# Optimization experiments

Measured on AMD Instinct MI355X. Metric: run time of the kernel, lower is better.

The kernel has to match this reference:

```python
import jax, jax.numpy as jnp
from jax import lax
import numpy as np

IOU_THRESHOLD = 0.35
SCORE_THRESHOLD = 0.5


def _pairwise_iou(b):
    # b: [N,4] boxes in (ymin, xmin, ymax, xmax) convention (tf boxes)
    y1, x1, y2, x2 = b[:, 0], b[:, 1], b[:, 2], b[:, 3]
    area = (y2 - y1) * (x2 - x1)
    iy1 = jnp.maximum(y1[:, None], y1[None, :])
    ix1 = jnp.maximum(x1[:, None], x1[None, :])
    iy2 = jnp.minimum(y2[:, None], y2[None, :])
    ix2 = jnp.minimum(x2[:, None], x2[None, :])
    inter = jnp.maximum(iy2 - iy1, 0.0) * jnp.maximum(ix2 - ix1, 0.0)
    union = area[:, None] + area[None, :] - inter
    return jnp.where(union > 0, inter / union, 0.0)  # [N,N]


def _nms_sample_image(scores, boxes, anchors_wh, num_samples):
    # scores [N], boxes [N,4], anchors_wh [N,2]
    N = scores.shape[0]
    order = jnp.argsort(-scores)  # descending by score, like tf NMS
    s = scores[order]
    b = boxes[order]
    a = anchors_wh[order]
    valid = s > SCORE_THRESHOLD
    iou = _pairwise_iou(b)  # [N,N] on score-sorted boxes
    idx = jnp.arange(N)

    # greedy suppression: box i kept iff valid and no earlier kept box overlaps > thr
    def step(keep, i):
        suppressed = jnp.any(keep & (idx < i) & (iou[i] > IOU_THRESHOLD))
        return keep.at[i].set(valid[i] & ~suppressed), None

    keep, _ = lax.scan(step, jnp.zeros(N, dtype=bool), idx)

    # gather kept entries in (descending-score) order, then pad/slice to num_samples
    rank = jnp.cumsum(keep) - 1  # output slot for each kept entry
    slot = jnp.where(keep, jnp.minimum(rank, num_samples), num_samples)
    vals = jnp.concatenate([s[:, None], b, a], axis=1)  # [N,7]
    out = jnp.zeros((num_samples + 1, 7), vals.dtype).at[slot].set(vals)
    return out[:num_samples]  # [num_samples, 7] = (score | box(4) | anchor_wh(2))


def reference(scores, boxes, anchors, num_samples):
    # scores [B,H,W,1], boxes [B,H,W,4], anchors [B,H,W,4] (last 2 chans = w,h)
    B = scores.shape[0]
    sc = scores.reshape(B, -1)
    bx = boxes.reshape(B, -1, 4)
    an = anchors[..., 2:].reshape(B, -1, 2)
    out = jax.vmap(lambda s, b, a: _nms_sample_image(s, b, a, num_samples))(sc, bx, an)
    return out  # [B, num_samples, 7]


def setup_inputs() -> dict:
    key = jax.random.key(0)
    k1, k2, k3, k4, k5 = jax.random.split(key, 5)
    B, H, W = 8, 64, 64
    scores = jax.random.uniform(k1, (B, H, W, 1), dtype=jnp.float32)
    # well-formed tf boxes: ymin<ymax, xmin<xmax in [0,1]
    ymin = jax.random.uniform(k2, (B, H, W, 1), dtype=jnp.float32) * 0.8
    xmin = jax.random.uniform(k3, (B, H, W, 1), dtype=jnp.float32) * 0.8
    hh = jax.random.uniform(k4, (B, H, W, 1), dtype=jnp.float32) * 0.18 + 0.02
    ww = jax.random.uniform(k5, (B, H, W, 1), dtype=jnp.float32) * 0.18 + 0.02
    boxes = jnp.concatenate([ymin, xmin, ymin + hh, xmin + ww], axis=-1)
    # anchors: [cy, cx, w, h]-style; only last two channels are used
    k6 = jax.random.fold_in(key, 6)
    anchors = jax.random.uniform(k6, (B, H, W, 4), dtype=jnp.float32) * 0.25 + 0.05
    return {"scores": scores, "boxes": boxes, "anchors": anchors, "num_samples": 300}
```

## Files before the change

### kernel.cpp

```cpp
#include <hip/hip_runtime.h>

static constexpr float kIouT = 0.35f;
static constexpr float kScoreT = 0.5f;
static constexpr int kMaxKeep = 512;

__device__ __forceinline__ float iou_f(const float4 a, const float4 b) {
  float areaA = __fmul_rn(a.z - a.x, a.w - a.y);
  float areaB = __fmul_rn(b.z - b.x, b.w - b.y);
  float iy1 = fmaxf(a.x, b.x);
  float ix1 = fmaxf(a.y, b.y);
  float iy2 = fminf(a.z, b.z);
  float ix2 = fminf(a.w, b.w);
  float dy = fmaxf(iy2 - iy1, 0.0f);
  float dx = fmaxf(ix2 - ix1, 0.0f);
  float inter = __fmul_rn(dy, dx);
  float uni = (areaA + areaB) - inter;
  return (uni > 0.0f) ? __fdiv_rn(inter, uni) : 0.0f;
}

__device__ __forceinline__ unsigned long long rdlane64(unsigned long long v,
                                                       int l) {
  unsigned lo = (unsigned)__builtin_amdgcn_readlane((int)(unsigned)v, l);
  unsigned hi = (unsigned)__builtin_amdgcn_readlane((int)(unsigned)(v >> 32), l);
  return ((unsigned long long)hi << 32) | lo;
}

__global__ __launch_bounds__(256)
void nms_rank_kernel(const float* __restrict__ scores,
                     const float4* __restrict__ boxes,
                     unsigned long long* __restrict__ skeys,
                     float4* __restrict__ sboxes,
                     int* __restrict__ Mcnt, int N, int rankBlocks) {
  const int tid = threadIdx.x;
  const int lane = tid & 63;
  if ((int)blockIdx.x >= rankBlocks) {
    __shared__ int part[4];
    const int img = blockIdx.x - rankBlocks;
    const int wv = tid >> 6;
    const float4* sc4 = (const float4*)(scores + (size_t)img * N);
    int c = 0;
    for (int q = tid; q < (N >> 2); q += 256) {
      float4 v = sc4[q];
      c += (v.x > kScoreT) + (v.y > kScoreT) + (v.z > kScoreT) + (v.w > kScoreT);
    }
#pragma unroll
    for (int off = 1; off < 64; off <<= 1) c += __shfl_xor(c, off, 64);
    if (lane == 0) part[wv] = c;
    __syncthreads();
    if (tid == 0) Mcnt[img] = part[0] + part[1] + part[2] + part[3];
    return;
  }
  const int wid = (int)(((unsigned)blockIdx.x * blockDim.x + tid) >> 6);
  const int img = wid / N;
  const int row = wid - img * N;
  const float* sc = scores + (size_t)img * N;
  const float si = sc[row];
  if (!(si > kScoreT)) return;
  const float4* sc4 = (const float4*)sc;
  int cnt = 0;
  for (int q = lane; q < (N >> 2); q += 64) {
    const float4 v = sc4[q];
    const int j = q << 2;
    cnt += (v.x > si) + (v.y > si) + (v.z > si) + (v.w > si);
    if (v.x == si && j < row) cnt++;
    if (v.y == si && j + 1 < row) cnt++;
    if (v.z == si && j + 2 < row) cnt++;
    if (v.w == si && j + 3 < row) cnt++;
  }
#pragma unroll
  for (int off = 1; off < 64; off <<= 1) cnt += __shfl_xor(cnt, off, 64);
  if (lane == 0) {
    skeys[(size_t)img * N + cnt] =
        ((unsigned long long)(~__float_as_uint(si)) << 32) | (unsigned)row;
    sboxes[(size_t)img * N + cnt] = boxes[(size_t)img * N + row];
  }
}

__global__ __launch_bounds__(256)
void nms_mask_kernel(const float4* __restrict__ sboxes,
                     const int* __restrict__ Mcnt,
                     unsigned long long* __restrict__ mask,
                     int N, int totalRows) {
  const int wid = (int)(((unsigned)blockIdx.x * blockDim.x + threadIdx.x) >> 6);
  const int lane = threadIdx.x & 63;
  if (wid >= totalRows) return;
  const int img = wid / N;
  const int row = wid - img * N;
  const int m = Mcnt[img];
  if (row >= m) return;
  const float4* sb = sboxes + (size_t)img * N;
  const float4 bi = sb[row];
  const int nw = (m + 63) >> 6;
  unsigned long long* mrow = mask + (size_t)wid * (size_t)(N >> 6);
  for (int w = row >> 6; w < nw; ++w) {
    int j = (w << 6) | lane;
    bool sup = false;
    if (j > row && j < m) sup = iou_f(bi, sb[j]) > kIouT;
    unsigned long long bm = __ballot(sup);
    if (lane == 0) mrow[w] = bm;
  }
}

__global__ __launch_bounds__(64)
void nms_scan_kernel(const unsigned long long* __restrict__ skeys,
                     const float4* __restrict__ sboxes,
                     const int* __restrict__ Mcnt,
                     const unsigned long long* __restrict__ mask,
                     const float* __restrict__ anchors,
                     float* __restrict__ out, int N, int NS) {
  __shared__ int keptlist[kMaxKeep];
  const int img = blockIdx.x;
  const int lane = threadIdx.x;
  int m = Mcnt[img];
  if (m > N) m = N;
  const int nw = (m + 63) >> 6;
  const int stride = N >> 6;
  const unsigned long long* mbase = mask + (size_t)img * (size_t)N * stride;
  const unsigned long long* kg = skeys + (size_t)img * N;
  const float4* sb = sboxes + (size_t)img * N;
  const float* an = anchors + (size_t)img * (size_t)N * 4;
  float* o = out + (size_t)img * NS * 7;

  int kept = 0;
  unsigned long long remv = 0ull;

  if (m > 0) {
    auto dgload = [&](int cc) -> unsigned long long {
      return (cc < nw) ? mbase[(size_t)((cc << 6) + lane) * stride + cc] : 0ull;
    };
    unsigned long long dg0 = dgload(0);
    unsigned long long dg1 = dgload(1);
    unsigned long long dg2 = dgload(2);

    for (int c = 0; c < nw && kept < NS; ++c) {
      const int cb = c << 6;
      unsigned long long local = rdlane64(remv, c);
      const int rem = m - cb;
      unsigned long long avail = ~local;
      if (rem < 64) avail &= (1ull << rem) - 1ull;
      unsigned long long keptbits = 0ull;
      while (avail != 0ull && kept < NS) {
        const int b = (int)__builtin_ctzll(avail);
        if (lane == 0) keptlist[kept] = cb + b;
        kept++;
        keptbits |= 1ull << b;
        const unsigned long long rc = rdlane64(dg0, b);
        local |= rc;
        avail &= ~local;
        avail &= ~(1ull << b);
      }
      dg0 = dg1; dg1 = dg2; dg2 = dgload(c + 3);
      const bool lok = (lane > c) && (lane < nw);
      while (keptbits != 0ull) {
        unsigned long long t[8];
        int bs[8];
#pragma unroll
        for (int k = 0; k < 8; ++k) {
          if (keptbits != 0ull) {
            bs[k] = (int)__builtin_ctzll(keptbits);
            keptbits &= keptbits - 1ull;
          } else {
            bs[k] = -1;
          }
        }
#pragma unroll
        for (int k = 0; k < 8; ++k)
          t[k] = (bs[k] >= 0 && lok)
                     ? mbase[(size_t)(cb + bs[k]) * stride + lane]
                     : 0ull;
#pragma unroll
        for (int k = 0; k < 8; ++k)
          if (bs[k] >= 0) remv |= t[k];
      }
    }
  }

  __syncthreads();
  for (int t = lane; t < kept; t += 64) {
    const int i = keptlist[t];
    const unsigned long long ki = kg[i];
    const float4 bi = sb[i];
    const unsigned idx = (unsigned)ki;
    float* row = o + t * 7;
    row[0] = __uint_as_float(~(unsigned)(ki >> 32));
    row[1] = bi.x; row[2] = bi.y; row[3] = bi.z; row[4] = bi.w;
    row[5] = an[idx * 4 + 2];
    row[6] = an[idx * 4 + 3];
  }
  for (int t = kept * 7 + lane; t < NS * 7; t += 64) o[t] = 0.0f;
}

__global__ __launch_bounds__(1024)
void nms_fused_kernel(const float* __restrict__ scores,
                      const float4* __restrict__ boxes,
                      const float* __restrict__ anchors,
                      float* __restrict__ out, int N, int NS) {
  __shared__ unsigned long long keys[4096];
  __shared__ int s_m;
  if (N > 4096) return;
  const int img = blockIdx.x;
  const int tid = threadIdx.x;
  const float* sc = scores + (size_t)img * N;
  const float4* bx = boxes + (size_t)img * N;
  if (tid == 0) s_m = 0;
  __syncthreads();
  int cnt = 0;
  for (int i = tid; i < N; i += blockDim.x) {
    float s = sc[i];
    keys[i] = ((unsigned long long)(~__float_as_uint(s)) << 32) | (unsigned)i;
    if (s > kScoreT) cnt++;
  }
  if (cnt) atomicAdd(&s_m, cnt);
  __syncthreads();
  for (int k = 2; k <= N; k <<= 1) {
    for (int j = k >> 1; j > 0; j >>= 1) {
      for (int i = tid; i < N; i += blockDim.x) {
        int ixj = i ^ j;
        if (ixj > i) {
          unsigned long long a = keys[i];
          unsigned long long b = keys[ixj];
          bool up = ((i & k) == 0);
          if (up ? (a > b) : (a < b)) { keys[i] = b; keys[ixj] = a; }
        }
      }
      __syncthreads();
    }
  }
  if (tid >= 64) return;
  const int lane = tid;
  const int m = s_m;
  const int nw = (m + 63) >> 6;
  const float* an = anchors + (size_t)img * N * 4;
  float* o = out + (size_t)img * NS * 7;
  unsigned long long remv = 0ull;
  int kept = 0;
  for (int i = 0; i < m && kept < NS; ++i) {
    unsigned long long rw = __shfl(remv, i >> 6, 64);
    if ((rw >> (i & 63)) & 1ull) continue;
    unsigned long long ki = keys[i];
    float4 bi = bx[(unsigned)ki];
    if (lane == 0) {
      unsigned idx = (unsigned)ki;
      float* row = o + kept * 7;
      row[0] = __uint_as_float(~(unsigned)(ki >> 32));
      row[1] = bi.x; row[2] = bi.y; row[3] = bi.z; row[4] = bi.w;
      row[5] = an[idx * 4 + 2];
      row[6] = an[idx * 4 + 3];
    }
    kept++;
    for (int w2 = i >> 6; w2 < nw; ++w2) {
      int j = (w2 << 6) | lane;
      bool sup = false;
      if (j > i && j < m) sup = iou_f(bi, bx[(unsigned)keys[j]]) > kIouT;
      unsigned long long bm = __ballot(sup);
      if (lane == w2) remv |= bm;
    }
  }
  for (int t = kept * 7 + lane; t < NS * 7; t += 64) o[t] = 0.0f;
}

extern "C" void kernel_launch(void* const* d_in, const int* in_sizes, int n_in,
                              void* d_out, int out_size, void* d_ws, size_t ws_size,
                              hipStream_t stream) {
  const float* scores = (const float*)d_in[0];
  const float4* boxes = (const float4*)d_in[1];
  const float* anchors = (const float*)d_in[2];
  float* out = (float*)d_out;
  const int B = 8;
  const int N = in_sizes[0] / B;
  const int NS = out_size / (B * 7);

  const size_t nTot = (size_t)B * (size_t)N;
  const size_t keysB = nTot * 8;
  const size_t sboxB = nTot * 16;
  const size_t mcntB = 256;
  const size_t maskB = nTot * (size_t)(N >> 6) * 8;
  const size_t need = keysB + sboxB + mcntB + maskB;

  if (ws_size >= need && (N % 256) == 0 && N >= 256 && N <= 4096 &&
      NS <= kMaxKeep) {
    char* p = (char*)d_ws;
    unsigned long long* skeys = (unsigned long long*)p; p += keysB;
    float4* sboxes = (float4*)p;                         p += sboxB;
    int* Mcnt = (int*)p;                                 p += mcntB;
    unsigned long long* mask = (unsigned long long*)p;

    const int totalRows = B * N;
    const int rankBlocks = totalRows / 4;
    nms_rank_kernel<<<rankBlocks + B, 256, 0, stream>>>(scores, boxes, skeys,
                                                        sboxes, Mcnt, N,
                                                        rankBlocks);
    nms_mask_kernel<<<rankBlocks, 256, 0, stream>>>(sboxes, Mcnt, mask, N,
                                                    totalRows);
    nms_scan_kernel<<<B, 64, 0, stream>>>(skeys, sboxes, Mcnt, mask, anchors,
                                          out, N, NS);
  } else {
    nms_fused_kernel<<<B, 1024, 0, stream>>>(scores, boxes, anchors, out, N, NS);
  }
}
```

Baseline: 108.2 us.

## Replace precomputed NMS mask with on-the-fly chunked suppression in one block per image

Drops the full pairwise IoU bitmask kernel and the mask-based scan, and adds a single 512-thread block per image. Each thread holds up to eight candidate boxes in registers. The block processes 64-box chunks: it resolves in-chunk suppression through a shared diagonal mask, then each thread tests its surviving boxes only against newly kept boxes. This removes the O(N^2) mask write and read traffic and one kernel launch, and stops early once NS boxes are kept. In exchange, the greedy scan is serialized through several block barriers per chunk. The IoU test also gains an early exit for boxes that do not intersect.

```diff
diff --git a/kernel.cpp b/kernel.cpp
--- a/kernel.cpp
+++ b/kernel.cpp
@@ -4,18 +4,16 @@
 static constexpr float kScoreT = 0.5f;
 static constexpr int kMaxKeep = 512;
 
-__device__ __forceinline__ float iou_f(const float4 a, const float4 b) {
-  float areaA = __fmul_rn(a.z - a.x, a.w - a.y);
-  float areaB = __fmul_rn(b.z - b.x, b.w - b.y);
-  float iy1 = fmaxf(a.x, b.x);
-  float ix1 = fmaxf(a.y, b.y);
-  float iy2 = fminf(a.z, b.z);
-  float ix2 = fminf(a.w, b.w);
-  float dy = fmaxf(iy2 - iy1, 0.0f);
-  float dx = fmaxf(ix2 - ix1, 0.0f);
-  float inter = __fmul_rn(dy, dx);
-  float uni = (areaA + areaB) - inter;
-  return (uni > 0.0f) ? __fdiv_rn(inter, uni) : 0.0f;
+__device__ __forceinline__ bool iou_gt(const float4 a, const float4 b) {
+  const float iy1 = fmaxf(a.x, b.x), ix1 = fmaxf(a.y, b.y);
+  const float iy2 = fminf(a.z, b.z), ix2 = fminf(a.w, b.w);
+  const float dy = iy2 - iy1, dx = ix2 - ix1;
+  if (!(dy > 0.0f && dx > 0.0f)) return false;
+  const float inter = __fmul_rn(dy, dx);
+  const float aA = __fmul_rn(a.z - a.x, a.w - a.y);
+  const float aB = __fmul_rn(b.z - b.x, b.w - b.y);
+  const float uni = (aA + aB) - inter;
+  return (uni > 0.0f) && (__fdiv_rn(inter, uni) > kIouT);
 }
 
 __device__ __forceinline__ unsigned long long rdlane64(unsigned long long v,
@@ -76,107 +74,111 @@
   }
 }
 
-__global__ __launch_bounds__(256)
-void nms_mask_kernel(const float4* __restrict__ sboxes,
-                     const int* __restrict__ Mcnt,
-                     unsigned long long* __restrict__ mask,
-                     int N, int totalRows) {
-  const int wid = (int)(((unsigned)blockIdx.x * blockDim.x + threadIdx.x) >> 6);
-  const int lane = threadIdx.x & 63;
-  if (wid >= totalRows) return;
-  const int img = wid / N;
-  const int row = wid - img * N;
-  const int m = Mcnt[img];
-  if (row >= m) return;
-  const float4* sb = sboxes + (size_t)img * N;
-  const float4 bi = sb[row];
-  const int nw = (m + 63) >> 6;
-  unsigned long long* mrow = mask + (size_t)wid * (size_t)(N >> 6);
-  for (int w = row >> 6; w < nw; ++w) {
-    int j = (w << 6) | lane;
-    bool sup = false;
-    if (j > row && j < m) sup = iou_f(bi, sb[j]) > kIouT;
-    unsigned long long bm = __ballot(sup);
-    if (lane == 0) mrow[w] = bm;
-  }
-}
-
-__global__ __launch_bounds__(64)
-void nms_scan_kernel(const unsigned long long* __restrict__ skeys,
+__global__ __launch_bounds__(512, 1)
+void nms_keep_kernel(const unsigned long long* __restrict__ skeys,
                      const float4* __restrict__ sboxes,
                      const int* __restrict__ Mcnt,
-                     const unsigned long long* __restrict__ mask,
                      const float* __restrict__ anchors,
                      float* __restrict__ out, int N, int NS) {
+  __shared__ float4 keptbox[kMaxKeep];
   __shared__ int keptlist[kMaxKeep];
+  __shared__ float4 chunkbox[64];
+  __shared__ unsigned long long smask[64];
+  __shared__ unsigned long long s_ca;
+  __shared__ int s_kept;
   const int img = blockIdx.x;
-  const int lane = threadIdx.x;
+  const int tid = threadIdx.x;
+  const int lane = tid & 63;
+  const int wv = tid >> 6;
   int m = Mcnt[img];
   if (m > N) m = N;
-  const int nw = (m + 63) >> 6;
-  const int stride = N >> 6;
-  const unsigned long long* mbase = mask + (size_t)img * (size_t)N * stride;
+  if (m < 0) m = 0;
   const unsigned long long* kg = skeys + (size_t)img * N;
   const float4* sb = sboxes + (size_t)img * N;
   const float* an = anchors + (size_t)img * (size_t)N * 4;
   float* o = out + (size_t)img * NS * 7;
 
+  float4 obox[8];
+  unsigned alivebits = 0u;
+#pragma unroll
+  for (int k = 0; k < 8; ++k) {
+    const int idx = tid + (k << 9);
+    if (idx < m) { obox[k] = sb[idx]; alivebits |= 1u << k; }
+  }
+  if (tid == 0) s_kept = 0;
+  __syncthreads();
+
   int kept = 0;
-  unsigned long long remv = 0ull;
-
-  if (m > 0) {
-    auto dgload = [&](int cc) -> unsigned long long {
-      return (cc < nw) ? mbase[(size_t)((cc << 6) + lane) * stride + cc] : 0ull;
-    };
-    unsigned long long dg0 = dgload(0);
-    unsigned long long dg1 = dgload(1);
-    unsigned long long dg2 = dgload(2);
-
-    for (int c = 0; c < nw && kept < NS; ++c) {
-      const int cb = c << 6;
-      unsigned long long local = rdlane64(remv, c);
-      const int rem = m - cb;
-      unsigned long long avail = ~local;
-      if (rem < 64) avail &= (1ull << rem) - 1ull;
-      unsigned long long keptbits = 0ull;
-      while (avail != 0ull && kept < NS) {
-        const int b = (int)__builtin_ctzll(avail);
-        if (lane == 0) keptlist[kept] = cb + b;
-        kept++;
-        keptbits |= 1ull << b;
-        const unsigned long long rc = rdlane64(dg0, b);
-        local |= rc;
-        avail &= ~local;
-        avail &= ~(1ull << b);
-      }
-      dg0 = dg1; dg1 = dg2; dg2 = dgload(c + 3);
-      const bool lok = (lane > c) && (lane < nw);
-      while (keptbits != 0ull) {
-        unsigned long long t[8];
-        int bs[8];
-#pragma unroll
-        for (int k = 0; k < 8; ++k) {
-          if (keptbits != 0ull) {
-            bs[k] = (int)__builtin_ctzll(keptbits);
-            keptbits &= keptbits - 1ull;
-          } else {
-            bs[k] = -1;
+  for (int base = 0; base < m && kept < NS; base += 64) {
+    const int ow = (base >> 6) & 7;
+    const int slot = base >> 9;
+    if (wv == ow) {
+      float4 cb = obox[0];
+#pragma unroll
+      for (int k = 1; k < 8; ++k)
+        if (k == slot) cb = obox[k];
+      chunkbox[lane] = cb;
+      const bool al = (alivebits >> slot) & 1u;
+      const unsigned long long bm = __ballot(al);
+      if (lane == 0) s_ca = bm;
+      alivebits &= ~(1u << slot);
+    }
+    __syncthreads();
+    const unsigned long long ca = s_ca;
+    if (ca != 0ull) {
+      const int kbase = kept;
+      {
+        const float4 cj = chunkbox[lane];
+#pragma unroll
+        for (int r = 0; r < 8; ++r) {
+          const int row = (wv << 3) + r;
+          const float4 bi = chunkbox[row];
+          bool sup = false;
+          if (lane > row) sup = iou_gt(bi, cj);
+          const unsigned long long bm = __ballot(sup);
+          if (lane == 0) smask[row] = bm;
+        }
+      }
+      __syncthreads();
+      if (wv == 0) {
+        const unsigned long long diag = smask[lane];
+        unsigned long long avail = ca;
+        unsigned long long local = 0ull, keptbits = 0ull;
+        int kc = kept;
+        while (avail != 0ull && kc < NS) {
+          const int b = (int)__builtin_ctzll(avail);
+          keptbits |= 1ull << b;
+          kc++;
+          local |= rdlane64(diag, b);
+          avail &= ~local;
+          avail &= ~(1ull << b);
+        }
+        if ((keptbits >> lane) & 1ull) {
+          const int rk =
+              (int)__builtin_popcountll(keptbits & ((1ull << lane) - 1ull));
+          keptlist[kbase + rk] = base + lane;
+          keptbox[kbase + rk] = chunkbox[lane];
+        }
+        if (lane == 0) s_kept = kc;
+      }
+      __syncthreads();
+      kept = s_kept;
+      if (kept > kbase && alivebits != 0u) {
+        for (int kk = kbase; kk < kept; ++kk) {
+          const float4 bx = keptbox[kk];
+#pragma unroll
+          for (int k = 0; k < 8; ++k) {
+            if ((alivebits >> k) & 1u) {
+              if (iou_gt(bx, obox[k])) alivebits &= ~(1u << k);
+            }
           }
         }
-#pragma unroll
-        for (int k = 0; k < 8; ++k)
-          t[k] = (bs[k] >= 0 && lok)
-                     ? mbase[(size_t)(cb + bs[k]) * stride + lane]
-                     : 0ull;
-#pragma unroll
-        for (int k = 0; k < 8; ++k)
-          if (bs[k] >= 0) remv |= t[k];
-      }
-    }
-  }
-
-  __syncthreads();
-  for (int t = lane; t < kept; t += 64) {
+      }
+    }
+    __syncthreads();
+  }
+
+  for (int t = tid; t < kept; t += 512) {
     const int i = keptlist[t];
     const unsigned long long ki = kg[i];
     const float4 bi = sb[i];
@@ -187,7 +189,7 @@
     row[5] = an[idx * 4 + 2];
     row[6] = an[idx * 4 + 3];
   }
-  for (int t = kept * 7 + lane; t < NS * 7; t += 64) o[t] = 0.0f;
+  for (int t = kept * 7 + tid; t < NS * 7; t += 512) o[t] = 0.0f;
 }
 
 __global__ __launch_bounds__(1024)
@@ -251,7 +253,7 @@
     for (int w2 = i >> 6; w2 < nw; ++w2) {
       int j = (w2 << 6) | lane;
       bool sup = false;
-      if (j > i && j < m) sup = iou_f(bi, bx[(unsigned)keys[j]]) > kIouT;
+      if (j > i && j < m) sup = iou_gt(bi, bx[(unsigned)keys[j]]);
       unsigned long long bm = __ballot(sup);
       if (lane == w2) remv |= bm;
     }
@@ -274,26 +276,22 @@
   const size_t keysB = nTot * 8;
   const size_t sboxB = nTot * 16;
   const size_t mcntB = 256;
-  const size_t maskB = nTot * (size_t)(N >> 6) * 8;
-  const size_t need = keysB + sboxB + mcntB + maskB;
+  const size_t need = keysB + sboxB + mcntB;
 
   if (ws_size >= need && (N % 256) == 0 && N >= 256 && N <= 4096 &&
       NS <= kMaxKeep) {
     char* p = (char*)d_ws;
     unsigned long long* skeys = (unsigned long long*)p; p += keysB;
     float4* sboxes = (float4*)p;                         p += sboxB;
-    int* Mcnt = (int*)p;                                 p += mcntB;
-    unsigned long long* mask = (unsigned long long*)p;
+    int* Mcnt = (int*)p;
 
     const int totalRows = B * N;
     const int rankBlocks = totalRows / 4;
     nms_rank_kernel<<<rankBlocks + B, 256, 0, stream>>>(scores, boxes, skeys,
                                                         sboxes, Mcnt, N,
                                                         rankBlocks);
-    nms_mask_kernel<<<rankBlocks, 256, 0, stream>>>(sboxes, Mcnt, mask, N,
-                                                    totalRows);
-    nms_scan_kernel<<<B, 64, 0, stream>>>(skeys, sboxes, Mcnt, mask, anchors,
-                                          out, N, NS);
+    nms_keep_kernel<<<B, 512, 0, stream>>>(skeys, sboxes, Mcnt, anchors, out,
+                                           N, NS);
   } else {
     nms_fused_kernel<<<B, 1024, 0, stream>>>(scores, boxes, anchors, out, N, NS);
   }
```

After: 248.0 us. +129.2%, slower.
